# Kernel tuning notes

Hardware: AMD Instinct MI355X
Metric: run time of the kernel (lower is better)

## Reference

```python
import jax, jax.numpy as jnp
import numpy as np

N_EMBD = 768
N_HEAD = 12
HEAD_DIM = N_EMBD // N_HEAD  # 64


def apply_rotary_emb(x, cos, sin):
    d = x.shape[-1] // 2
    x1, x2 = x[..., :d], x[..., d:]
    y1 = x1 * cos + x2 * sin
    y2 = x1 * -sin + x2 * cos
    return jnp.concatenate([y1, y2], axis=-1)


def rms_norm(x):
    return x * jax.lax.rsqrt(jnp.mean(jnp.square(x), axis=-1, keepdims=True) + 1e-06)


def setup_inputs() -> dict:
    key = jax.random.key(0)
    ks = jax.random.split(key, 7)
    B, T = 2, 2048
    x = jax.random.normal(ks[0], (B, T, N_EMBD), dtype=jnp.float32)
    # cos/sin broadcast over (B, head) axes of [B, T, H, HEAD_DIM//2]
    cos = jax.random.uniform(ks[1], (T, 1, HEAD_DIM // 2), dtype=jnp.float32)
    sin = jax.random.uniform(ks[2], (T, 1, HEAD_DIM // 2), dtype=jnp.float32)
    scale = 1.0 / np.sqrt(N_EMBD)
    wq = jax.random.normal(ks[3], (N_EMBD, N_EMBD), dtype=jnp.float32) * scale
    wk = jax.random.normal(ks[4], (N_EMBD, N_EMBD), dtype=jnp.float32) * scale
    wv = jax.random.normal(ks[5], (N_EMBD, N_EMBD), dtype=jnp.float32) * scale
    wproj = jax.random.normal(ks[6], (N_EMBD, N_EMBD), dtype=jnp.float32) * scale
    return {"x": x, "cos": cos, "sin": sin, "wq": wq, "wk": wk, "wv": wv, "wproj": wproj}


def reference(x, cos, sin, wq, wk, wv, wproj):
    B, T, C = x.shape
    q = (x @ wq).reshape(B, T, N_HEAD, HEAD_DIM)
    k = (x @ wk).reshape(B, T, N_HEAD, HEAD_DIM)
    v = (x @ wv).reshape(B, T, N_HEAD, HEAD_DIM)
    q = rms_norm(apply_rotary_emb(q, cos, sin))
    k = rms_norm(apply_rotary_emb(k, cos, sin))
    # [B, H, T, T] attention scores (non-causal, as in source)
    attn = jnp.einsum('bqhd,bkhd->bhqk', q, k) / jnp.sqrt(jnp.float32(HEAD_DIM))
    attn = jax.nn.softmax(attn, axis=-1)
    y = jnp.einsum('bhqk,bkhd->bqhd', attn, v).reshape(B, T, C)
    return y @ wproj
```

## Files before the change

### kernel.cpp

```cpp
#include <hip/hip_runtime.h>
#include <hip/hip_bf16.h>
#include <stdint.h>

typedef __attribute__((ext_vector_type(8))) __bf16 bf16x8;
typedef __attribute__((ext_vector_type(4))) __bf16 bf16x4;
typedef __attribute__((ext_vector_type(2))) __bf16 bf16x2;
typedef __attribute__((ext_vector_type(4))) float f32x4;
typedef __attribute__((ext_vector_type(16))) float f32x16;
typedef __attribute__((ext_vector_type(8))) unsigned short u16x8;
typedef __attribute__((ext_vector_type(4))) unsigned int u32x4;

#define DEVI __device__ __forceinline__

DEVI void gload16(const void* g, void* l) {
  __builtin_amdgcn_global_load_lds((const __attribute__((address_space(1))) void*)g,
                                   (__attribute__((address_space(3))) void*)l, 16, 0, 0);
}

DEVI uint32_t pack2(float a, float b) {
  bf16x2 t;
  t[0] = (__bf16)a;
  t[1] = (__bf16)b;
  return __builtin_bit_cast(uint32_t, t);
}

DEVI int vswz(int d) { return ((d ^ (d >> 3)) & 7) << 4; }

__global__ __launch_bounds__(256) void cvt_x_k(const float* __restrict__ x,
                                               __bf16* __restrict__ xb, int n4) {
  int i = blockIdx.x * blockDim.x + threadIdx.x;
  int stride = gridDim.x * blockDim.x;
  for (; i < n4; i += stride) {
    float4 v = ((const float4*)x)[i];
    bf16x4 o;
    o[0] = (__bf16)v.x; o[1] = (__bf16)v.y; o[2] = (__bf16)v.z; o[3] = (__bf16)v.w;
    ((bf16x4*)xb)[i] = o;
  }
}

__global__ __launch_bounds__(256) void wtrans_k(const float* __restrict__ wq,
                                                const float* __restrict__ wk,
                                                const float* __restrict__ wv,
                                                const float* __restrict__ wp,
                                                __bf16* __restrict__ WT) {
  __shared__ float tile[32][33];
  const float* W = (blockIdx.z == 0) ? wq : (blockIdx.z == 1) ? wk : (blockIdx.z == 2) ? wv : wp;
  int n0 = blockIdx.x * 32, k0 = blockIdx.y * 32;
  int tx = threadIdx.x, ty = threadIdx.y;
#pragma unroll
  for (int j = 0; j < 4; ++j)
    tile[ty + 8 * j][tx] = W[(size_t)(k0 + ty + 8 * j) * 768 + n0 + tx];
  __syncthreads();
#pragma unroll
  for (int j = 0; j < 4; ++j)
    WT[(size_t)(blockIdx.z * 768 + n0 + ty + 8 * j) * 768 + k0 + tx] =
        (__bf16)tile[tx][ty + 8 * j];
}

template <int EPI, int BN>
__global__ __launch_bounds__(256) void gemm_k(const __bf16* __restrict__ A,
                                              const __bf16* __restrict__ B,
                                              void* __restrict__ Cout,
                                              const float* __restrict__ cosT,
                                              const float* __restrict__ sinT,
                                              int K, int lda, int ldb, int ldc,
                                              int nwg, int nxb) {
  constexpr int NF = BN / 32;
  constexpr int LPT = 2 + BN / 64;
  __shared__ __align__(16) __bf16 Al[4][128 * 32];
  __shared__ __align__(16) __bf16 Bl[4][BN * 32];
  const int tid = threadIdx.x, lane = tid & 63, w = tid >> 6;
  const int wm = w >> 1, wn = w & 1;
  const int bid = blockIdx.x;
  const int o = (bid & 7) * (nwg >> 3) + (bid >> 3);
  const int bx = o % nxb, by = o / nxb;
  const int m0 = by * 128, n0 = bx * BN;
  const int c = lane & 15, g = lane >> 4;
  f32x4 acc[4][NF] = {};

  auto stage = [&](int k0, int buf) {
#pragma unroll
    for (int i = 0; i < 2; ++i) {
      int e = (i * 256 + tid) * 8;
      int row = e >> 5, col = e & 31;
      gload16(A + (size_t)(m0 + row) * lda + k0 + col, (char*)&Al[buf][0] + 2 * (size_t)e);
    }
#pragma unroll
    for (int i = 0; i < BN / 64; ++i) {
      int e = (i * 256 + tid) * 8;
      int row = e >> 5, col = e & 31;
      gload16(B + (size_t)(n0 + row) * ldb + k0 + col, (char*)&Bl[buf][0] + 2 * (size_t)e);
    }
  };

  const int NIT = K / 32;
  stage(0, 0);
  stage(32, 1);
  for (int t = 0; t < NIT; ++t) {
    if (t + 2 < NIT) {
      stage((t + 2) * 32, (t + 2) & 3);
      asm volatile("s_waitcnt vmcnt(%0)" ::"i"(2 * LPT) : "memory");
    } else if (t + 1 < NIT) {
      asm volatile("s_waitcnt vmcnt(%0)" ::"i"(LPT) : "memory");
    } else {
      asm volatile("s_waitcnt vmcnt(0)" ::: "memory");
    }
    __builtin_amdgcn_s_barrier();
    const int cur = t & 3;
    bf16x8 af[4], bfr[NF];
#pragma unroll
    for (int q = 0; q < 4; ++q)
      af[q] = *(const bf16x8*)&Al[cur][(wm * 64 + q * 16 + c) * 32 + 8 * g];
#pragma unroll
    for (int q = 0; q < NF; ++q)
      bfr[q] = *(const bf16x8*)&Bl[cur][(wn * (BN / 2) + q * 16 + c) * 32 + 8 * g];
#pragma unroll
    for (int mf = 0; mf < 4; ++mf)
#pragma unroll
      for (int nf = 0; nf < NF; ++nf)
        acc[mf][nf] = __builtin_amdgcn_mfma_f32_16x16x32_bf16(af[mf], bfr[nf],
                                                              acc[mf][nf], 0, 0, 0);
  }

  if (EPI == 1) {
    __bf16* out = (__bf16*)Cout;
    const int colbase = n0 + wn * 64;
    const int plane = colbase / 768;
#pragma unroll
    for (int mf = 0; mf < 4; ++mf) {
#pragma unroll
      for (int r = 0; r < 4; ++r) {
        int row = m0 + wm * 64 + mf * 16 + 4 * g + r;
        float v0 = acc[mf][0][r], v1 = acc[mf][1][r], v2 = acc[mf][2][r], v3 = acc[mf][3][r];
        float y0, y1, y2, y3;
        if (plane < 2) {
          int t = row & 2047;
          float c0 = cosT[t * 32 + c],      s0 = sinT[t * 32 + c];
          float c1 = cosT[t * 32 + 16 + c], s1 = sinT[t * 32 + 16 + c];
          y0 = v0 * c0 + v2 * s0;
          y2 = v2 * c0 - v0 * s0;
          y1 = v1 * c1 + v3 * s1;
          y3 = v3 * c1 - v1 * s1;
          float ss = y0 * y0 + y1 * y1 + y2 * y2 + y3 * y3;
          ss += __shfl_xor(ss, 1); ss += __shfl_xor(ss, 2);
          ss += __shfl_xor(ss, 4); ss += __shfl_xor(ss, 8);
          float rn = rsqrtf(ss * (1.0f / 64.0f) + 1e-6f);
          y0 *= rn; y1 *= rn; y2 *= rn; y3 *= rn;
        } else {
          y0 = v0; y1 = v1; y2 = v2; y3 = v3;
        }
        size_t base = (size_t)row * ldc + colbase + c;
        out[base +  0] = (__bf16)y0;
        out[base + 16] = (__bf16)y1;
        out[base + 32] = (__bf16)y2;
        out[base + 48] = (__bf16)y3;
      }
    }
  } else {
    float* out = (float*)Cout;
#pragma unroll
    for (int mf = 0; mf < 4; ++mf)
#pragma unroll
      for (int nf = 0; nf < NF; ++nf)
#pragma unroll
        for (int r = 0; r < 4; ++r) {
          int row = m0 + wm * 64 + mf * 16 + 4 * g + r;
          out[(size_t)row * ldc + n0 + wn * (BN / 2) + nf * 16 + c] = acc[mf][nf][r];
        }
  }
}

__global__ __launch_bounds__(128) void attn_k(const __bf16* __restrict__ QKV,
                                              __bf16* __restrict__ Yb) {
  constexpr int TT = 2048, KVB = 64, NT = TT / KVB;
  __shared__ __align__(16) char smem[32768];
  const int tid = threadIdx.x, lane = tid & 63, w = tid >> 6;
  const int q5 = lane & 31, h = lane >> 5;
  const int bid = blockIdx.x;
  const int xcd = bid & 7, idx = bid >> 3;
  const int bh = xcd * 3 + (idx >> 5), qb = idx & 31;
  const int b = bh / 12, hd = bh % 12;
  const size_t ldq = 2304;
  const __bf16* Qg = QKV + (size_t)(b * TT) * ldq + hd * 64;
  const __bf16* Kg = QKV + (size_t)(b * TT) * ldq + 768 + hd * 64;
  const __bf16* Vg = QKV + (size_t)(b * TT) * ldq + 1536 + hd * 64;

  const int qrow = qb * 64 + w * 32 + q5;
  bf16x8 aq[4];
#pragma unroll
  for (int t = 0; t < 4; ++t)
    aq[t] = *(const bf16x8*)(Qg + (size_t)qrow * ldq + t * 16 + 8 * h);

  u16x8 vr[4];
  auto stageK = [&](int kv0, int buf) {
#pragma unroll
    for (int p = 0; p < 4; ++p) {
      int cid = p * 128 + tid;
      int row = cid >> 3, s = cid & 7;
      int srccol = 8 * (s ^ (row & 7));
      gload16(Kg + (size_t)(kv0 + row) * ldq + srccol,
              smem + buf * 8192 + row * 128 + 16 * s);
    }
  };
  auto loadV = [&](int kv0) {
#pragma unroll
    for (int p = 0; p < 2; ++p) {
      int u = p * 128 + tid;
      int kp = u >> 3, d0 = (u & 7) * 8;
      const __bf16* src0 = Vg + (size_t)(kv0 + 2 * kp) * ldq + d0;
      vr[2 * p] = *(const u16x8*)src0;
      vr[2 * p + 1] = *(const u16x8*)(src0 + ldq);
    }
  };
  auto writeV = [&](int buf) {
    char* vb = smem + 16384 + buf * 8192;
#pragma unroll
    for (int p = 0; p < 2; ++p) {
      int u = p * 128 + tid;
      int kp = u >> 3, d0 = (u & 7) * 8;
#pragma unroll
      for (int i = 0; i < 8; ++i) {
        int d = d0 + i;
        int byte = (d * 128 + 4 * kp) ^ vswz(d);
        uint32_t pk = (uint32_t)vr[2 * p][i] | ((uint32_t)vr[2 * p + 1][i] << 16);
        *(uint32_t*)(vb + byte) = pk;
      }
    }
  };

  f32x16 Yacc[2] = {};
  const float SC = 0.18033688f;
  float m2 = -__builtin_inff(), l_run = 0.f;

  stageK(0, 0);
  loadV(0);
  writeV(0);
  __syncthreads();

  for (int t = 0; t < NT; ++t) {
    const int cur = t & 1;
    const char* Kb = smem + cur * 8192;
    const char* Vb = smem + 16384 + cur * 8192;
    if (t + 1 < NT) {
      stageK((t + 1) * KVB, cur ^ 1);
      loadV((t + 1) * KVB);
    }

    f32x16 Sv[2];
#pragma unroll
    for (int j = 0; j < 2; ++j) {
      f32x16 S = {};
#pragma unroll
      for (int tt = 0; tt < 4; ++tt) {
        int row = j * 32 + q5;
        int chunk = (2 * tt + h) ^ (q5 & 7);
        bf16x8 kf = *(const bf16x8*)(Kb + row * 128 + 16 * chunk);
        S = __builtin_amdgcn_mfma_f32_32x32x16_bf16(kf, aq[tt], S, 0, 0, 0);
      }
      Sv[j] = S;
    }
#define SV(i) Sv[(i) >> 4][(i) & 15]

    float m0 = SV(0), m1 = SV(1), m2c = SV(2), m3 = SV(3);
#pragma unroll
    for (int i = 4; i < 32; i += 4) {
      m0 = fmaxf(m0, SV(i));     m1 = fmaxf(m1, SV(i + 1));
      m2c = fmaxf(m2c, SV(i + 2)); m3 = fmaxf(m3, SV(i + 3));
    }
    float mx = fmaxf(fmaxf(m0, m1), fmaxf(m2c, m3));
    mx = fmaxf(mx, __shfl_xor(mx, 32));
    mx *= SC;
    if (!__all(mx <= m2 + 8.0f)) {
      float mn = fmaxf(m2, mx);
      float corr = __builtin_exp2f(m2 - mn);
      l_run *= corr;
#pragma unroll
      for (int dh = 0; dh < 2; ++dh)
#pragma unroll
        for (int r = 0; r < 16; ++r) Yacc[dh][r] *= corr;
      m2 = mn;
    }
    float rs0 = 0.f, rs1 = 0.f, rs2 = 0.f, rs3 = 0.f;
#pragma unroll
    for (int i = 0; i < 32; i += 4) {
      float e0 = __builtin_exp2f(fmaf(SV(i), SC, -m2));
      float e1 = __builtin_exp2f(fmaf(SV(i + 1), SC, -m2));
      float e2 = __builtin_exp2f(fmaf(SV(i + 2), SC, -m2));
      float e3 = __builtin_exp2f(fmaf(SV(i + 3), SC, -m2));
      SV(i) = e0; SV(i + 1) = e1; SV(i + 2) = e2; SV(i + 3) = e3;
      rs0 += e0; rs1 += e1; rs2 += e2; rs3 += e3;
    }
    float rs = (rs0 + rs1) + (rs2 + rs3);
    rs += __shfl_xor(rs, 32);
    l_run += rs;

#pragma unroll
    for (int j = 0; j < 2; ++j) {
#pragma unroll
      for (int s = 0; s < 2; ++s) {
        int e0 = j * 16 + s * 8;
        uint32_t pk01 = pack2(SV(e0 + 0), SV(e0 + 1));
        uint32_t pk23 = pack2(SV(e0 + 2), SV(e0 + 3));
        uint32_t pk45 = pack2(SV(e0 + 4), SV(e0 + 5));
        uint32_t pk67 = pack2(SV(e0 + 6), SV(e0 + 7));
        uint32_t fa = (uint32_t)__shfl_xor((int)(h ? pk01 : pk45), 32);
        uint32_t fb = (uint32_t)__shfl_xor((int)(h ? pk23 : pk67), 32);
        u32x4 pw;
        pw[0] = h ? fa : pk01;
        pw[1] = h ? fb : pk23;
        pw[2] = h ? pk45 : fa;
        pw[3] = h ? pk67 : fb;
        bf16x8 pfrag = __builtin_bit_cast(bf16x8, pw);
        int keyb = j * 64 + s * 32 + 16 * h;
#pragma unroll
        for (int dh = 0; dh < 2; ++dh) {
          int d = dh * 32 + q5;
          int byte = (d * 128 + keyb) ^ vswz(d);
          bf16x8 vf = *(const bf16x8*)(Vb + byte);
          Yacc[dh] = __builtin_amdgcn_mfma_f32_32x32x16_bf16(vf, pfrag, Yacc[dh], 0, 0, 0);
        }
      }
    }
#undef SV
    if (t + 1 < NT) writeV(cur ^ 1);
    __syncthreads();
  }

  float rl = __builtin_amdgcn_rcpf(l_run);
  char* yb = smem + w * (32 * 144);
#pragma unroll
  for (int dh = 0; dh < 2; ++dh)
#pragma unroll
    for (int a = 0; a < 4; ++a) {
      bf16x4 pkv;
#pragma unroll
      for (int i = 0; i < 4; ++i) pkv[i] = (__bf16)(Yacc[dh][a * 4 + i] * rl);
      int d0 = a * 8 + 4 * h + 32 * dh;
      *(bf16x4*)(yb + q5 * 144 + d0 * 2) = pkv;
    }
  __syncthreads();
  __bf16* Yrow = Yb + (size_t)(b * TT + qb * 64 + w * 32) * 768 + hd * 64;
#pragma unroll
  for (int k = 0; k < 4; ++k) {
    int chunk = k * 64 + lane;
    int qr = chunk >> 3, sr = chunk & 7;
    bf16x8 vv = *(const bf16x8*)(yb + qr * 144 + sr * 16);
    *(bf16x8*)(Yrow + (size_t)qr * 768 + sr * 8) = vv;
  }
}

extern "C" void kernel_launch(void* const* d_in, const int* in_sizes, int n_in,
                              void* d_out, int out_size, void* d_ws, size_t ws_size,
                              hipStream_t stream) {
  const float* x = (const float*)d_in[0];
  const float* cosT = (const float*)d_in[1];
  const float* sinT = (const float*)d_in[2];
  const float* wq = (const float*)d_in[3];
  const float* wk = (const float*)d_in[4];
  const float* wv = (const float*)d_in[5];
  const float* wp = (const float*)d_in[6];

  char* ws = (char*)d_ws;
  __bf16* xb   = (__bf16*)(ws);
  __bf16* WT   = (__bf16*)(ws + 6291456);
  __bf16* QKVb = (__bf16*)(ws + 11010048);
  __bf16* Yb   = (__bf16*)(ws + 29884416);

  cvt_x_k<<<2048, 256, 0, stream>>>(x, xb, (4096 * 768) / 4);
  wtrans_k<<<dim3(24, 24, 4), dim3(32, 8), 0, stream>>>(wq, wk, wv, wp, WT);
  gemm_k<1, 128><<<576, 256, 0, stream>>>(xb, WT, (void*)QKVb, cosT, sinT,
                                          768, 768, 768, 2304, 576, 18);
  attn_k<<<768, 128, 0, stream>>>(QKVb, Yb);
  gemm_k<0, 64><<<384, 256, 0, stream>>>(Yb, WT + (size_t)2304 * 768, d_out,
                                         nullptr, nullptr, 768, 768, 768, 768, 384, 12);
}
```

Baseline: 212.1 us.

## Fuse prep kernels and restructure attention with 128-key tiles and direct K loads

Merges the x conversion and weight-transpose kernels into a single prep launch to cut launch overhead. In attention, the KV tile grows from 64 to 128 keys, halving loop iterations and barriers. K fragments are now read straight from global memory into registers instead of being staged through LDS, and the freed LDS holds a double-buffered 128-key V tile with a wider swizzle. This raises register pressure (16 K fragments, 4 score tiles, 8 V regs) and makes the K reads less coalesced, relying on cache hits instead.

```diff
diff --git a/kernel.cpp b/kernel.cpp
--- a/kernel.cpp
+++ b/kernel.cpp
@@ -24,37 +24,41 @@
   return __builtin_bit_cast(uint32_t, t);
 }
 
-DEVI int vswz(int d) { return ((d ^ (d >> 3)) & 7) << 4; }
-
-__global__ __launch_bounds__(256) void cvt_x_k(const float* __restrict__ x,
-                                               __bf16* __restrict__ xb, int n4) {
-  int i = blockIdx.x * blockDim.x + threadIdx.x;
-  int stride = gridDim.x * blockDim.x;
-  for (; i < n4; i += stride) {
-    float4 v = ((const float4*)x)[i];
-    bf16x4 o;
-    o[0] = (__bf16)v.x; o[1] = (__bf16)v.y; o[2] = (__bf16)v.z; o[3] = (__bf16)v.w;
-    ((bf16x4*)xb)[i] = o;
-  }
-}
-
-__global__ __launch_bounds__(256) void wtrans_k(const float* __restrict__ wq,
-                                                const float* __restrict__ wk,
-                                                const float* __restrict__ wv,
-                                                const float* __restrict__ wp,
-                                                __bf16* __restrict__ WT) {
+DEVI int vswz(int d) { return ((d ^ (d >> 3)) & 15) << 4; }
+
+__global__ __launch_bounds__(256) void prep_k(const float* __restrict__ x,
+                                              const float* __restrict__ wq,
+                                              const float* __restrict__ wk,
+                                              const float* __restrict__ wv,
+                                              const float* __restrict__ wp,
+                                              __bf16* __restrict__ xb,
+                                              __bf16* __restrict__ WT) {
   __shared__ float tile[32][33];
-  const float* W = (blockIdx.z == 0) ? wq : (blockIdx.z == 1) ? wk : (blockIdx.z == 2) ? wv : wp;
-  int n0 = blockIdx.x * 32, k0 = blockIdx.y * 32;
-  int tx = threadIdx.x, ty = threadIdx.y;
-#pragma unroll
-  for (int j = 0; j < 4; ++j)
-    tile[ty + 8 * j][tx] = W[(size_t)(k0 + ty + 8 * j) * 768 + n0 + tx];
-  __syncthreads();
-#pragma unroll
-  for (int j = 0; j < 4; ++j)
-    WT[(size_t)(blockIdx.z * 768 + n0 + ty + 8 * j) * 768 + k0 + tx] =
-        (__bf16)tile[tx][ty + 8 * j];
+  const int bid = blockIdx.x, tid = threadIdx.x;
+  if (bid < 2304) {
+    const int z = bid / 576, r = bid % 576;
+    const int bx = r % 24, by = r / 24;
+    const float* W = (z == 0) ? wq : (z == 1) ? wk : (z == 2) ? wv : wp;
+    int n0 = bx * 32, k0 = by * 32;
+    int tx = tid & 31, ty = tid >> 5;
+#pragma unroll
+    for (int j = 0; j < 4; ++j)
+      tile[ty + 8 * j][tx] = W[(size_t)(k0 + ty + 8 * j) * 768 + n0 + tx];
+    __syncthreads();
+#pragma unroll
+    for (int j = 0; j < 4; ++j)
+      WT[(size_t)(z * 768 + n0 + ty + 8 * j) * 768 + k0 + tx] =
+          (__bf16)tile[tx][ty + 8 * j];
+  } else {
+    const int n4 = (4096 * 768) / 4;
+    int i = (bid - 2304) * 256 + tid;
+    for (; i < n4; i += 768 * 256) {
+      float4 v = ((const float4*)x)[i];
+      bf16x4 o;
+      o[0] = (__bf16)v.x; o[1] = (__bf16)v.y; o[2] = (__bf16)v.z; o[3] = (__bf16)v.w;
+      ((bf16x4*)xb)[i] = o;
+    }
+  }
 }
 
 template <int EPI, int BN>
@@ -172,7 +176,7 @@
 
 __global__ __launch_bounds__(128) void attn_k(const __bf16* __restrict__ QKV,
                                               __bf16* __restrict__ Yb) {
-  constexpr int TT = 2048, KVB = 64, NT = TT / KVB;
+  constexpr int TT = 2048, KVB = 128, NT = TT / KVB;
   __shared__ __align__(16) char smem[32768];
   const int tid = threadIdx.x, lane = tid & 63, w = tid >> 6;
   const int q5 = lane & 31, h = lane >> 5;
@@ -191,20 +195,10 @@
   for (int t = 0; t < 4; ++t)
     aq[t] = *(const bf16x8*)(Qg + (size_t)qrow * ldq + t * 16 + 8 * h);
 
-  u16x8 vr[4];
-  auto stageK = [&](int kv0, int buf) {
+  u16x8 vr[8];
+  auto loadV = [&](int kv0) {
 #pragma unroll
     for (int p = 0; p < 4; ++p) {
-      int cid = p * 128 + tid;
-      int row = cid >> 3, s = cid & 7;
-      int srccol = 8 * (s ^ (row & 7));
-      gload16(Kg + (size_t)(kv0 + row) * ldq + srccol,
-              smem + buf * 8192 + row * 128 + 16 * s);
-    }
-  };
-  auto loadV = [&](int kv0) {
-#pragma unroll
-    for (int p = 0; p < 2; ++p) {
       int u = p * 128 + tid;
       int kp = u >> 3, d0 = (u & 7) * 8;
       const __bf16* src0 = Vg + (size_t)(kv0 + 2 * kp) * ldq + d0;
@@ -213,15 +207,15 @@
     }
   };
   auto writeV = [&](int buf) {
-    char* vb = smem + 16384 + buf * 8192;
-#pragma unroll
-    for (int p = 0; p < 2; ++p) {
+    char* vb = smem + buf * 16384;
+#pragma unroll
+    for (int p = 0; p < 4; ++p) {
       int u = p * 128 + tid;
       int kp = u >> 3, d0 = (u & 7) * 8;
 #pragma unroll
       for (int i = 0; i < 8; ++i) {
         int d = d0 + i;
-        int byte = (d * 128 + 4 * kp) ^ vswz(d);
+        int byte = (d * 256 + 4 * kp) ^ vswz(d);
         uint32_t pk = (uint32_t)vr[2 * p][i] | ((uint32_t)vr[2 * p + 1][i] << 16);
         *(uint32_t*)(vb + byte) = pk;
       }
@@ -232,39 +226,39 @@
   const float SC = 0.18033688f;
   float m2 = -__builtin_inff(), l_run = 0.f;
 
-  stageK(0, 0);
   loadV(0);
   writeV(0);
   __syncthreads();
 
+  f32x16 Sv[4];
+#define SV(i) Sv[(i) >> 4][(i) & 15]
+
   for (int t = 0; t < NT; ++t) {
     const int cur = t & 1;
-    const char* Kb = smem + cur * 8192;
-    const char* Vb = smem + 16384 + cur * 8192;
-    if (t + 1 < NT) {
-      stageK((t + 1) * KVB, cur ^ 1);
-      loadV((t + 1) * KVB);
-    }
-
-    f32x16 Sv[2];
-#pragma unroll
-    for (int j = 0; j < 2; ++j) {
+    const int kv0 = t * KVB;
+    const char* Vb = smem + cur * 16384;
+    if (t + 1 < NT) loadV(kv0 + KVB);
+
+    bf16x8 kf[4][4];
+#pragma unroll
+    for (int j = 0; j < 4; ++j)
+#pragma unroll
+      for (int tt = 0; tt < 4; ++tt)
+        kf[j][tt] = *(const bf16x8*)(Kg + (size_t)(kv0 + j * 32 + q5) * ldq + tt * 16 + 8 * h);
+
+#pragma unroll
+    for (int j = 0; j < 4; ++j) {
       f32x16 S = {};
 #pragma unroll
-      for (int tt = 0; tt < 4; ++tt) {
-        int row = j * 32 + q5;
-        int chunk = (2 * tt + h) ^ (q5 & 7);
-        bf16x8 kf = *(const bf16x8*)(Kb + row * 128 + 16 * chunk);
-        S = __builtin_amdgcn_mfma_f32_32x32x16_bf16(kf, aq[tt], S, 0, 0, 0);
-      }
+      for (int tt = 0; tt < 4; ++tt)
+        S = __builtin_amdgcn_mfma_f32_32x32x16_bf16(kf[j][tt], aq[tt], S, 0, 0, 0);
       Sv[j] = S;
     }
-#define SV(i) Sv[(i) >> 4][(i) & 15]
 
     float m0 = SV(0), m1 = SV(1), m2c = SV(2), m3 = SV(3);
 #pragma unroll
-    for (int i = 4; i < 32; i += 4) {
-      m0 = fmaxf(m0, SV(i));     m1 = fmaxf(m1, SV(i + 1));
+    for (int i = 4; i < 64; i += 4) {
+      m0 = fmaxf(m0, SV(i));       m1 = fmaxf(m1, SV(i + 1));
       m2c = fmaxf(m2c, SV(i + 2)); m3 = fmaxf(m3, SV(i + 3));
     }
     float mx = fmaxf(fmaxf(m0, m1), fmaxf(m2c, m3));
@@ -282,7 +276,7 @@
     }
     float rs0 = 0.f, rs1 = 0.f, rs2 = 0.f, rs3 = 0.f;
 #pragma unroll
-    for (int i = 0; i < 32; i += 4) {
+    for (int i = 0; i < 64; i += 4) {
       float e0 = __builtin_exp2f(fmaf(SV(i), SC, -m2));
       float e1 = __builtin_exp2f(fmaf(SV(i + 1), SC, -m2));
       float e2 = __builtin_exp2f(fmaf(SV(i + 2), SC, -m2));
@@ -295,7 +289,7 @@
     l_run += rs;
 
 #pragma unroll
-    for (int j = 0; j < 2; ++j) {
+    for (int j = 0; j < 4; ++j) {
 #pragma unroll
       for (int s = 0; s < 2; ++s) {
         int e0 = j * 16 + s * 8;
@@ -315,16 +309,16 @@
 #pragma unroll
         for (int dh = 0; dh < 2; ++dh) {
           int d = dh * 32 + q5;
-          int byte = (d * 128 + keyb) ^ vswz(d);
+          int byte = (d * 256 + keyb) ^ vswz(d);
           bf16x8 vf = *(const bf16x8*)(Vb + byte);
           Yacc[dh] = __builtin_amdgcn_mfma_f32_32x32x16_bf16(vf, pfrag, Yacc[dh], 0, 0, 0);
         }
       }
     }
-#undef SV
     if (t + 1 < NT) writeV(cur ^ 1);
     __syncthreads();
   }
+#undef SV
 
   float rl = __builtin_amdgcn_rcpf(l_run);
   char* yb = smem + w * (32 * 144);
@@ -366,8 +360,7 @@
   __bf16* QKVb = (__bf16*)(ws + 11010048);
   __bf16* Yb   = (__bf16*)(ws + 29884416);
 
-  cvt_x_k<<<2048, 256, 0, stream>>>(x, xb, (4096 * 768) / 4);
-  wtrans_k<<<dim3(24, 24, 4), dim3(32, 8), 0, stream>>>(wq, wk, wv, wp, WT);
+  prep_k<<<3072, 256, 0, stream>>>(x, wq, wk, wv, wp, xb, WT);
   gemm_k<1, 128><<<576, 256, 0, stream>>>(xb, WT, (void*)QKVb, cosT, sinT,
                                           768, 768, 768, 2304, 576, 18);
   attn_k<<<768, 128, 0, stream>>>(QKVb, Yb);
```

After: 269.1 us. 26.8% more time.
